# Kernel optimization log

Hardware: AMD Instinct MI355X
Metric: run time of the kernel (lower is better)

Reference implementation:

```python
import jax, jax.numpy as jnp
import numpy as np

B, D, OUT = 256, 512, 1024
H = (D + 1) * D // 2  # 131328 packed upper-triangular features


def setup_inputs() -> dict:
    key = jax.random.key(0)
    k1, k2 = jax.random.split(key)
    x = jax.random.normal(k1, (B, D), dtype=jnp.float32)
    # Linear weight [out_dim, halfway_dim]; original inits to zeros (learned param),
    # use small random values so the baseline output is nontrivial. bias=False.
    W = jax.random.normal(k2, (OUT, H), dtype=jnp.float32) * 0.02
    return {"x": x, "W": W}


def reference(x, W):
    d = x.shape[-1]
    iu, ju = jnp.triu_indices(d)            # static upper-tri indices (incl. diagonal)
    outer = jnp.einsum('bi,bj->bij', x, x)  # [B, D, D] per-sample outer product
    packed = outer[:, iu, ju]               # [B, H] triu gather (row-major order, matches torch bool mask)
    return packed @ W.T                     # [B, OUT] Linear, no bias
```

## Files before the change

### kernel.cpp

```cpp
#include <hip/hip_runtime.h>
#include <hip/hip_bf16.h>


#define DDIM 512
#define ODIM 1024
#define HDIM 131328L
#define NSPLIT 32
#define AST 40
#define WST 40

typedef __attribute__((ext_vector_type(4))) float floatx4;
typedef __attribute__((ext_vector_type(8))) short short8;
typedef floatx4 __attribute__((aligned(4))) floatx4u;

__device__ inline floatx4 load4u(const float* p) { return *(const floatx4u*)p; }

__device__ inline unsigned short f2bf(float v) {
    return __builtin_bit_cast(unsigned short, __float2bfloat16(v));
}

__device__ inline unsigned f2bf2(float a, float b) {
    return (unsigned)f2bf(a) | ((unsigned)f2bf(b) << 16);
}

#define BAR_PLAIN() asm volatile("s_barrier" ::: "memory")
#define BAR_LGKM()  asm volatile("s_waitcnt lgkmcnt(0)\n\ts_barrier" ::: "memory")

__global__ __launch_bounds__(512, 2) void selmul_kernel(const float* __restrict__ x,
                                                        const float* __restrict__ W,
                                                        float* __restrict__ part) {
    __shared__ __align__(16) unsigned short A_lds[256 * AST];
    __shared__ __align__(16) unsigned short W_lds[128 * WST];

    const int t    = threadIdx.x;
    const int lane = t & 63;
    const int wave = t >> 6;
    const int wm   = (wave >> 1) * 64;
    const int wn   = (wave & 1) * 64;
    const int l15  = lane & 15;
    const int quad = lane >> 4;

    const int n0 = blockIdx.x * 128;
    const int s  = blockIdx.y;

    const int c4 = t & 7;
    const int rv = t >> 3;

    floatx4 acc[4][4] = {};
    floatx4 av[4], wv[2];
    float   xi[4];

    auto mfma_phase = [&]() {
        short8 af[4], bw[4];
        #pragma unroll
        for (int fm = 0; fm < 4; ++fm)
            af[fm] = *(const short8*)&A_lds[(wm + fm * 16 + l15) * AST + quad * 8];
        #pragma unroll
        for (int fn = 0; fn < 4; ++fn)
            bw[fn] = *(const short8*)&W_lds[(wn + fn * 16 + l15) * WST + quad * 8];
        #pragma unroll
        for (int fm = 0; fm < 4; ++fm)
            #pragma unroll
            for (int fn = 0; fn < 4; ++fn)
                acc[fm][fn] = __builtin_amdgcn_mfma_f32_16x16x32_bf16(
                    af[fm], bw[fn], acc[fm][fn], 0, 0, 0);
    };

    for (int tseg = 0; tseg < 16; ++tseg) {
        const int tt   = tseg >> 1;
        const int i    = (tseg & 1) ? (63 - s + 64 * tt) : (s + 64 * tt);
        const int len  = DDIM - i;
        const long base = (long)i * DDIM - (long)i * (i - 1) / 2;
        const int full = len >> 5;
        const int rem  = len & 31;

        #pragma unroll
        for (int e = 0; e < 4; ++e)
            xi[e] = x[(rv + 64 * e) * DDIM + i];

        if (full > 0) {
            const float* axp = x + rv * DDIM + i + c4 * 4;
            const float* wpp = W + (long)(n0 + rv) * HDIM + base + c4 * 4;
            #pragma unroll
            for (int e = 0; e < 4; ++e) av[e] = load4u(axp + e * 64 * DDIM);
            #pragma unroll
            for (int e = 0; e < 2; ++e) wv[e] = load4u(wpp + (long)e * 64 * HDIM);
            axp += 32; wpp += 32;

            for (int st = 0; st < full; ++st) {
                BAR_PLAIN();
                #pragma unroll
                for (int e = 0; e < 4; ++e) {
                    const int row = rv + 64 * e;
                    floatx4 v = av[e];
                    const float sc = xi[e];
                    uint2 p;
                    p.x = f2bf2(v.x * sc, v.y * sc);
                    p.y = f2bf2(v.z * sc, v.w * sc);
                    *(uint2*)&A_lds[row * AST + c4 * 4] = p;
                }
                #pragma unroll
                for (int e = 0; e < 2; ++e) {
                    const int row = rv + 64 * e;
                    floatx4 v = wv[e];
                    uint2 p;
                    p.x = f2bf2(v.x, v.y);
                    p.y = f2bf2(v.z, v.w);
                    *(uint2*)&W_lds[row * WST + c4 * 4] = p;
                }
                if (st + 1 < full) {
                    #pragma unroll
                    for (int e = 0; e < 4; ++e) av[e] = load4u(axp + e * 64 * DDIM);
                    #pragma unroll
                    for (int e = 0; e < 2; ++e) wv[e] = load4u(wpp + (long)e * 64 * HDIM);
                    axp += 32; wpp += 32;
                }
                BAR_LGKM();
                mfma_phase();
            }
        }

        if (rem) {
            const int jj = t & 31;
            const int rb = t >> 5;
            const int j0 = i + full * 32;
            const bool valid = jj < rem;
            const int j = valid ? (j0 + jj) : i;
            const long kc = base + (long)full * 32;
            BAR_PLAIN();
            #pragma unroll
            for (int e = 0; e < 16; ++e) {
                const int m = rb + 16 * e;
                float a = valid ? x[m * DDIM + j] * x[m * DDIM + i] : 0.0f;
                A_lds[m * AST + jj] = f2bf(a);
            }
            #pragma unroll
            for (int e = 0; e < 8; ++e) {
                const int n = rb + 16 * e;
                const long ks = valid ? (kc + jj) : base;
                W_lds[n * WST + jj] = f2bf(W[(long)(n0 + n) * HDIM + ks]);
            }
            BAR_LGKM();
            mfma_phase();
        }
    }

    float* po = part + (long)s * (256 * ODIM);
    #pragma unroll
    for (int fm = 0; fm < 4; ++fm) {
        const int row = wm + fm * 16 + quad * 4;
        #pragma unroll
        for (int fn = 0; fn < 4; ++fn) {
            const int col = n0 + wn + fn * 16 + l15;
            #pragma unroll
            for (int r = 0; r < 4; ++r)
                po[(row + r) * ODIM + col] = acc[fm][fn][r];
        }
    }
}

__global__ __launch_bounds__(256) void reduce_kernel(const float* __restrict__ part,
                                                     float* __restrict__ out) {
    const int gid = blockIdx.x * 256 + threadIdx.x;
    floatx4 acc = {};
    #pragma unroll
    for (int sp = 0; sp < NSPLIT; ++sp) {
        floatx4 v = *(const floatx4*)(part + (long)sp * (256 * ODIM) + gid * 4);
        acc += v;
    }
    *(floatx4*)(out + gid * 4) = acc;
}

extern "C" void kernel_launch(void* const* d_in, const int* in_sizes, int n_in,
                              void* d_out, int out_size, void* d_ws, size_t ws_size,
                              hipStream_t stream) {
    const float* x = (const float*)d_in[0];
    const float* W = (const float*)d_in[1];
    float* out  = (float*)d_out;
    float* part = (float*)d_ws;

    hipLaunchKernelGGL(selmul_kernel, dim3(8, NSPLIT), dim3(512), 0, stream, x, W, part);
    hipLaunchKernelGGL(reduce_kernel, dim3(256), dim3(256), 0, stream, part, out);
}
```

Baseline: 854.6 us.

## Double split-K count, prefetch W two steps ahead, and multi-accumulator reduce

Raises the split-K factor from 32 to 64 so the grid has 512 blocks with half as many triangle rows each, and raises launch-bound occupancy to 4 blocks per CU. The W global loads are double-buffered two steps ahead to hide more HBM latency. The reduce kernel uses four independent accumulators. In exchange it doubles the partial-sum workspace and reduce traffic, and the tighter register budget may cause spills.

Measured after the change: 1.046 ms. 22.4% more time.

```diff
diff --git a/kernel.cpp b/kernel.cpp
--- a/kernel.cpp
+++ b/kernel.cpp
@@ -5,7 +5,7 @@
 #define DDIM 512
 #define ODIM 1024
 #define HDIM 131328L
-#define NSPLIT 32
+#define NSPLIT 64
 #define AST 40
 #define WST 40
 
@@ -26,7 +26,7 @@
 #define BAR_PLAIN() asm volatile("s_barrier" ::: "memory")
 #define BAR_LGKM()  asm volatile("s_waitcnt lgkmcnt(0)\n\ts_barrier" ::: "memory")
 
-__global__ __launch_bounds__(512, 2) void selmul_kernel(const float* __restrict__ x,
+__global__ __launch_bounds__(512, 4) void selmul_kernel(const float* __restrict__ x,
                                                         const float* __restrict__ W,
                                                         float* __restrict__ part) {
     __shared__ __align__(16) unsigned short A_lds[256 * AST];
@@ -47,7 +47,7 @@
     const int rv = t >> 3;
 
     floatx4 acc[4][4] = {};
-    floatx4 av[4], wv[2];
+    floatx4 av[4], wvA[2], wvB[2];
     float   xi[4];
 
     auto mfma_phase = [&]() {
@@ -66,9 +66,9 @@
                     af[fm], bw[fn], acc[fm][fn], 0, 0, 0);
     };
 
-    for (int tseg = 0; tseg < 16; ++tseg) {
+    for (int tseg = 0; tseg < 8; ++tseg) {
         const int tt   = tseg >> 1;
-        const int i    = (tseg & 1) ? (63 - s + 64 * tt) : (s + 64 * tt);
+        const int i    = (tseg & 1) ? (127 - s + 128 * tt) : (s + 128 * tt);
         const int len  = DDIM - i;
         const long base = (long)i * DDIM - (long)i * (i - 1) / 2;
         const int full = len >> 5;
@@ -84,10 +84,14 @@
             #pragma unroll
             for (int e = 0; e < 4; ++e) av[e] = load4u(axp + e * 64 * DDIM);
             #pragma unroll
-            for (int e = 0; e < 2; ++e) wv[e] = load4u(wpp + (long)e * 64 * HDIM);
-            axp += 32; wpp += 32;
+            for (int e = 0; e < 2; ++e) wvA[e] = load4u(wpp + (long)e * 64 * HDIM);
+            if (full > 1) {
+                #pragma unroll
+                for (int e = 0; e < 2; ++e) wvB[e] = load4u(wpp + 32 + (long)e * 64 * HDIM);
+            }
+            axp += 32; wpp += 64;
 
-            for (int st = 0; st < full; ++st) {
+            auto step_body = [&](floatx4 (&wvp)[2], int st) {
                 BAR_PLAIN();
                 #pragma unroll
                 for (int e = 0; e < 4; ++e) {
@@ -102,7 +106,7 @@
                 #pragma unroll
                 for (int e = 0; e < 2; ++e) {
                     const int row = rv + 64 * e;
-                    floatx4 v = wv[e];
+                    floatx4 v = wvp[e];
                     uint2 p;
                     p.x = f2bf2(v.x, v.y);
                     p.y = f2bf2(v.z, v.w);
@@ -111,12 +115,20 @@
                 if (st + 1 < full) {
                     #pragma unroll
                     for (int e = 0; e < 4; ++e) av[e] = load4u(axp + e * 64 * DDIM);
+                    axp += 32;
+                }
+                if (st + 2 < full) {
                     #pragma unroll
-                    for (int e = 0; e < 2; ++e) wv[e] = load4u(wpp + (long)e * 64 * HDIM);
-                    axp += 32; wpp += 32;
+                    for (int e = 0; e < 2; ++e) wvp[e] = load4u(wpp + (long)e * 64 * HDIM);
+                    wpp += 32;
                 }
                 BAR_LGKM();
                 mfma_phase();
+            };
+
+            for (int st = 0; st < full; st += 2) {
+                step_body(wvA, st);
+                if (st + 1 < full) step_body(wvB, st + 1);
             }
         }
 
@@ -162,13 +174,15 @@
 __global__ __launch_bounds__(256) void reduce_kernel(const float* __restrict__ part,
                                                      float* __restrict__ out) {
     const int gid = blockIdx.x * 256 + threadIdx.x;
-    floatx4 acc = {};
+    floatx4 a0 = {}, a1 = {}, a2 = {}, a3 = {};
     #pragma unroll
-    for (int sp = 0; sp < NSPLIT; ++sp) {
-        floatx4 v = *(const floatx4*)(part + (long)sp * (256 * ODIM) + gid * 4);
-        acc += v;
+    for (int sp = 0; sp < NSPLIT; sp += 4) {
+        a0 += *(const floatx4*)(part + (long)(sp + 0) * (256 * ODIM) + gid * 4);
+        a1 += *(const floatx4*)(part + (long)(sp + 1) * (256 * ODIM) + gid * 4);
+        a2 += *(const floatx4*)(part + (long)(sp + 2) * (256 * ODIM) + gid * 4);
+        a3 += *(const floatx4*)(part + (long)(sp + 3) * (256 * ODIM) + gid * 4);
     }
-    *(floatx4*)(out + gid * 4) = acc;
+    *(floatx4*)(out + gid * 4) = (a0 + a1) + (a2 + a3);
 }
 
 extern "C" void kernel_launch(void* const* d_in, const int* in_sizes, int n_in,
```
